# Kernel tuning notes

Measured on AMD Instinct MI355X. Metric: run time of the kernel, lower is better.

## Reference

```python
import jax, jax.numpy as jnp
import numpy as np

B, M, D, H, F, N = 8, 1024, 1024, 16, 4096, 4
DK = D // H
EPS = 1e-5


def _ln(x, g, b):
    mu = jnp.mean(x, axis=-1, keepdims=True)
    var = jnp.mean(jnp.square(x - mu), axis=-1, keepdims=True)
    return (x - mu) * jax.lax.rsqrt(var + EPS) * g + b


def setup_inputs() -> dict:
    key = jax.random.key(0)
    ks = jax.random.split(key, 12)
    s = 0.02
    return {
        "embeds": jax.random.normal(ks[0], (B, M, D), dtype=jnp.float32),
        "weights": jax.random.normal(ks[1], (B, M), dtype=jnp.float32) * 0.1,
        "Wq": jax.random.normal(ks[2], (N, D, D), dtype=jnp.float32) * s,
        "bq": jnp.zeros((N, D), dtype=jnp.float32),
        "Wk": jax.random.normal(ks[3], (N, D, D), dtype=jnp.float32) * s,
        "bk": jnp.zeros((N, D), dtype=jnp.float32),
        "Wv": jax.random.normal(ks[4], (N, D, D), dtype=jnp.float32) * s,
        "bv": jnp.zeros((N, D), dtype=jnp.float32),
        "Wo": jax.random.normal(ks[5], (N, D, D), dtype=jnp.float32) * s,
        "bo": jnp.zeros((N, D), dtype=jnp.float32),
        "W1": jax.random.normal(ks[6], (N, D, F), dtype=jnp.float32) * s,
        "b1": jnp.zeros((N, F), dtype=jnp.float32),
        "W2": jax.random.normal(ks[7], (N, F, D), dtype=jnp.float32) * s,
        "b2": jnp.zeros((N, D), dtype=jnp.float32),
        "g1": jnp.ones((N, D), dtype=jnp.float32),
        "be1": jnp.zeros((N, D), dtype=jnp.float32),
        "g2": jnp.ones((N, D), dtype=jnp.float32),
        "be2": jnp.zeros((N, D), dtype=jnp.float32),
    }


def reference(embeds, weights, Wq, bq, Wk, bk, Wv, bv, Wo, bo,
              W1, b1, W2, b2, g1, be1, g2, be2):
    scale = 1.0 / np.sqrt(DK).astype(np.float32)
    bias = weights[:, None, None, :]  # b,1,1,m additive bias over keys

    def layer(x, p):
        wq, bq_, wk, bk_, wv, bv_, wo, bo_, w1, b1_, w2, b2_, g1_, be1_, g2_, be2_ = p
        q = (x @ wq + bq_).reshape(B, M, H, DK)
        k = (x @ wk + bk_).reshape(B, M, H, DK)
        v = (x @ wv + bv_).reshape(B, M, H, DK)
        scores = jnp.einsum("bqhd,bkhd->bhqk", q, k) * scale + bias
        attn = jax.nn.softmax(scores, axis=-1)
        o = jnp.einsum("bhqk,bkhd->bqhd", attn, v).reshape(B, M, D)
        o = o @ wo + bo_
        x = _ln(x + o, g1_, be1_)
        y = jax.nn.gelu(x @ w1 + b1_, approximate=False) @ w2 + b2_
        x = _ln(x + y, g2_, be2_)
        return x, None

    params = (Wq, bq, Wk, bk, Wv, bv, Wo, bo, W1, b1, W2, b2, g1, be1, g2, be2)
    out, _ = jax.lax.scan(layer, embeds, params)
    return out
```

## Files before the change

kernel.cpp:

```cpp
#include <hip/hip_runtime.h>
#include <hip/hip_bf16.h>

#define BB  8
#define MM  1024
#define DD  1024
#define HH  16
#define FF  4096
#define NL  4
#define DKK 64

typedef __bf16 bf16_t;
typedef __bf16 bf16x8 __attribute__((ext_vector_type(8)));
typedef __bf16 bf16x4 __attribute__((ext_vector_type(4)));
typedef float  f32x4  __attribute__((ext_vector_type(4)));

__device__ __forceinline__ void gld16(const bf16_t* g, bf16_t* l) {
    __builtin_amdgcn_global_load_lds((const __attribute__((address_space(1))) void*)g,
                                     (__attribute__((address_space(3))) void*)l,
                                     16, 0, 0);
}

__global__ __launch_bounds__(256) void cvt_x(const float* __restrict__ e,
                                             float* __restrict__ x,
                                             bf16_t* __restrict__ xb) {
    size_t i = ((size_t)blockIdx.x * 256 + threadIdx.x) * 4;
    float4 v = *(const float4*)(e + i);
    *(float4*)(x + i) = v;
    bf16x4 o;
    o[0] = (bf16_t)v.x; o[1] = (bf16_t)v.y; o[2] = (bf16_t)v.z; o[3] = (bf16_t)v.w;
    *(bf16x4*)(xb + i) = o;
}

__global__ __launch_bounds__(256) void transpose_all(const float* __restrict__ Wq,
                                                     const float* __restrict__ Wk,
                                                     const float* __restrict__ Wv,
                                                     const float* __restrict__ Wo,
                                                     const float* __restrict__ W1,
                                                     const float* __restrict__ W2,
                                                     bf16_t* __restrict__ qkvT,
                                                     bf16_t* __restrict__ WoT,
                                                     bf16_t* __restrict__ W1T,
                                                     bf16_t* __restrict__ W2T) {
    __shared__ float tile[32][33];
    const int bx = blockIdx.x;
    const float* in;
    bf16_t* out;
    int C, t;
    if (bx < 4096) {
        const int mat = bx >> 10;
        t = bx & 1023;
        C = 1024;
        in  = mat == 0 ? Wq : mat == 1 ? Wk : mat == 2 ? Wv : Wo;
        out = mat < 3 ? qkvT + (size_t)mat * DD * DD : WoT;
    } else if (bx < 8192) {
        t = bx - 4096; C = 4096; in = W1; out = W1T;
    } else {
        t = bx - 8192; C = 1024; in = W2; out = W2T;
    }
    const int cb = C >> 5;
    const int c0 = (t % cb) * 32, r0 = (t / cb) * 32;
    const int R = (C == 1024) ? ((bx < 8192) ? 1024 : 4096) : 1024;
    const int tx = threadIdx.x & 31, ty = threadIdx.x >> 5;
    for (int i = 0; i < 4; i++)
        tile[ty + i * 8][tx] = in[(size_t)(r0 + ty + i * 8) * C + c0 + tx];
    __syncthreads();
    for (int i = 0; i < 4; i++)
        out[(size_t)(c0 + ty + i * 8) * R + r0 + tx] = (bf16_t)tile[tx][ty + i * 8];
}

__global__ __launch_bounds__(256) void concat_bias(const float* __restrict__ bq,
                                                   const float* __restrict__ bk,
                                                   const float* __restrict__ bv,
                                                   float* __restrict__ out) {
    const int seg = blockIdx.x, l = blockIdx.y, t = threadIdx.x;
    const float* src = seg == 0 ? bq : seg == 1 ? bk : bv;
    float4 v = *(const float4*)(src + (size_t)l * 1024 + t * 4);
    *(float4*)(out + (size_t)l * 3072 + seg * 1024 + t * 4) = v;
}

__global__ __launch_bounds__(256) void transpose_v_k(const bf16_t* __restrict__ v,
                                                     bf16_t* __restrict__ vT, int ld) {
    __shared__ bf16_t t[64][65];
    int bh = blockIdx.y, b = bh >> 4, h = bh & 15;
    int m0 = blockIdx.x * 64;
    int tx = threadIdx.x & 63, ty = threadIdx.x >> 6;
    for (int i = 0; i < 16; i++) {
        int mr = ty * 16 + i;
        t[mr][tx] = v[(size_t)(b * MM + m0 + mr) * ld + h * DKK + tx];
    }
    __syncthreads();
    for (int i = 0; i < 16; i++) {
        int dk = ty * 16 + i;
        vT[((size_t)(bh * DKK + dk)) * MM + m0 + tx] = t[tx][dk];
    }
}

__device__ __forceinline__ void stage_plane(const bf16_t* __restrict__ G, int K,
                                            size_t rbase, size_t kcol0,
                                            bf16_t* lds, int w, int srow, int scol) {
#pragma unroll
    for (int j = 0; j < 2; j++)
        gld16(G + (rbase + (size_t)(j * 128 + w * 16 + srow)) * (size_t)K + kcol0 + scol,
              lds + j * 4096 + w * 512);
}

template <int EPI>
__global__ __launch_bounds__(512, 2) void gemm256(const bf16_t* __restrict__ A,
                                                  const bf16_t* __restrict__ Bt,
                                                  const float* __restrict__ bias,
                                                  const float* __restrict__ res,
                                                  bf16_t* __restrict__ outb,
                                                  float* __restrict__ outf,
                                                  int K, int Ntot) {
    __shared__ __align__(16) bf16_t As[2 * 2 * 256 * 32];
    __shared__ __align__(16) bf16_t Bs[2 * 2 * 256 * 32];
    const int tid = threadIdx.x, w = tid >> 6, lane = tid & 63;
    const int fr = lane & 15, quad = lane >> 4;
    const int wm = w >> 2, wn = w & 3;
    const int srow = lane >> 2;
    const int scol = ((lane & 3) ^ ((lane >> 3) & 3)) << 3;
    const int swz  = (quad ^ ((fr >> 1) & 3)) << 3;

    const int gx = gridDim.x;
    int lid = blockIdx.y * gx + blockIdx.x;
    {
        const int nwg = gx * gridDim.y;
        const int qq = nwg >> 3, rr = nwg & 7, xc = lid & 7, lq = lid >> 3;
        lid = (xc < rr ? xc * (qq + 1) : rr * (qq + 1) + (xc - rr) * qq) + lq;
    }
    const size_t bm = (size_t)(lid / gx) * 256;
    const size_t bn = (size_t)(lid % gx) * 256;

    const int NT = K >> 6;
    f32x4 acc[8][4] = {};

    stage_plane(A,  K, bm, 0,  As,         w, srow, scol);
    stage_plane(Bt, K, bn, 0,  Bs,         w, srow, scol);
    stage_plane(A,  K, bm, 32, As + 8192,  w, srow, scol);
    stage_plane(Bt, K, bn, 32, Bs + 8192,  w, srow, scol);
    stage_plane(A,  K, bm, 64, As + 16384, w, srow, scol);
    stage_plane(Bt, K, bn, 64, Bs + 16384, w, srow, scol);
    asm volatile("s_waitcnt vmcnt(8)\n\ts_barrier" ::: "memory");

    auto phase = [&](int rdbase, int stbase, size_t stk) {
        bf16x8 af[8], bfv[4];
        const bf16_t* Ap = As + rdbase;
        const bf16_t* Bp = Bs + rdbase;
#pragma unroll
        for (int i = 0; i < 8; i++)
            af[i] = *(const bf16x8*)&Ap[(wm * 128 + i * 16 + fr) * 32 + swz];
#pragma unroll
        for (int j = 0; j < 4; j++)
            bfv[j] = *(const bf16x8*)&Bp[(wn * 64 + j * 16 + fr) * 32 + swz];
        stage_plane(A,  K, bm, stk, As + stbase, w, srow, scol);
        stage_plane(Bt, K, bn, stk, Bs + stbase, w, srow, scol);
        asm volatile("s_barrier" ::: "memory");
        __builtin_amdgcn_s_setprio(1);
#pragma unroll
        for (int i = 0; i < 8; i++)
#pragma unroll
            for (int j = 0; j < 4; j++)
                acc[i][j] = __builtin_amdgcn_mfma_f32_16x16x32_bf16(af[i], bfv[j],
                                                                    acc[i][j], 0, 0, 0);
        __builtin_amdgcn_s_setprio(0);
        asm volatile("s_waitcnt vmcnt(8)\n\ts_barrier" ::: "memory");
    };

    for (int t = 0; t < NT; t += 2) {
        const size_t t1 = (t + 1 < NT) ? t + 1 : NT - 1;
        const size_t t2 = (t + 2 < NT) ? t + 2 : NT - 1;
        const size_t t3 = (t + 3 < NT) ? t + 3 : NT - 1;
        phase(0,     24576, t1 * 64 + 32);
        phase(8192,  0,     t2 * 64);
        phase(16384, 8192,  t2 * 64 + 32);
        phase(24576, 16384, t3 * 64);
    }

#pragma unroll
    for (int j = 0; j < 4; j++) {
        const size_t c = bn + wn * 64 + j * 16 + fr;
        const float bv = bias[c];
#pragma unroll
        for (int i = 0; i < 8; i++) {
            const size_t rbase = bm + wm * 128 + i * 16 + quad * 4;
#pragma unroll
            for (int r = 0; r < 4; r++) {
                const size_t idx = (rbase + r) * (size_t)Ntot + c;
                float v = acc[i][j][r] + bv;
                if constexpr (EPI == 0) {
                    outb[idx] = (bf16_t)v;
                } else if constexpr (EPI == 1) {
                    outf[idx] = v + res[idx];
                } else {
                    float g = 0.5f * v * (1.0f + erff(v * 0.70710678118654752f));
                    outb[idx] = (bf16_t)g;
                }
            }
        }
    }
}

__global__ __launch_bounds__(256) void flash_attn(const bf16_t* __restrict__ q,
                                                  const bf16_t* __restrict__ kmat,
                                                  const bf16_t* __restrict__ vT,
                                                  const float* __restrict__ wts,
                                                  bf16_t* __restrict__ ao, int ldq) {
    __shared__ bf16_t Ks[128 * 72];
    __shared__ bf16_t Vs[64 * 136];
    bf16_t* Ps = Ks;

    const int tid = threadIdx.x;
    const int wave = tid >> 6, lane = tid & 63;
    const int fr = lane & 15, quad = lane >> 4;
    const int fk = quad * 8;
    const int bh = blockIdx.y, b = bh >> 4, h = bh & 15;
    const int q0 = blockIdx.x * 64;

    const size_t qrow = (size_t)(b * MM + q0 + wave * 16 + fr) * ldq + h * DKK;
    const bf16x8 aq0 = *(const bf16x8*)(q + qrow + fk);
    const bf16x8 aq1 = *(const bf16x8*)(q + qrow + 32 + fk);

    f32x4 oacc[4] = {};
    float lrow[4] = {0.f, 0.f, 0.f, 0.f};

    for (int kt = 0; kt < MM; kt += 128) {
        __syncthreads();
#pragma unroll
        for (int rr = 0; rr < 4; rr++) {
            const int key = rr * 32 + (tid >> 3);
            const int dkc = (tid & 7) * 8;
            *(bf16x8*)(&Ks[key * 72 + dkc]) =
                *(const bf16x8*)(kmat + (size_t)(b * MM + kt + key) * ldq + h * DKK + dkc);
            const int dkr = rr * 16 + (tid >> 4);
            const int kc = (tid & 15) * 8;
            *(bf16x8*)(&Vs[dkr * 136 + kc]) =
                *(const bf16x8*)(vT + (size_t)(bh * DKK + dkr) * MM + kt + kc);
        }
        __syncthreads();

        f32x4 s[8];
#pragma unroll
        for (int ni = 0; ni < 8; ni++) {
            const bf16_t* kp = &Ks[(ni * 16 + fr) * 72];
            f32x4 z = {0.f, 0.f, 0.f, 0.f};
            z = __builtin_amdgcn_mfma_f32_16x16x32_bf16(aq0, *(const bf16x8*)(kp + fk), z, 0, 0, 0);
            z = __builtin_amdgcn_mfma_f32_16x16x32_bf16(aq1, *(const bf16x8*)(kp + 32 + fk), z, 0, 0, 0);
            const float wv = wts[b * MM + kt + ni * 16 + fr];
#pragma unroll
            for (int r = 0; r < 4; r++) s[ni][r] = __expf(z[r] * 0.125f + wv);
        }

        float rs[4] = {0.f, 0.f, 0.f, 0.f};
#pragma unroll
        for (int ni = 0; ni < 8; ni++)
#pragma unroll
            for (int r = 0; r < 4; r++) rs[r] += s[ni][r];
#pragma unroll
        for (int off = 1; off < 16; off <<= 1)
#pragma unroll
            for (int r = 0; r < 4; r++) rs[r] += __shfl_xor(rs[r], off, 16);
#pragma unroll
        for (int r = 0; r < 4; r++) lrow[r] += rs[r];

        __syncthreads();

#pragma unroll
        for (int ni = 0; ni < 8; ni++)
#pragma unroll
            for (int r = 0; r < 4; r++)
                Ps[(wave * 16 + quad * 4 + r) * 136 + ni * 16 + fr] = (bf16_t)s[ni][r];

#pragma unroll
        for (int c2 = 0; c2 < 4; c2++) {
            const bf16x8 ap = *(const bf16x8*)(&Ps[(wave * 16 + fr) * 136 + c2 * 32 + fk]);
#pragma unroll
            for (int ni = 0; ni < 4; ni++) {
                const bf16x8 bv = *(const bf16x8*)(&Vs[(ni * 16 + fr) * 136 + c2 * 32 + fk]);
                oacc[ni] = __builtin_amdgcn_mfma_f32_16x16x32_bf16(ap, bv, oacc[ni], 0, 0, 0);
            }
        }
    }

    const size_t orow = (size_t)(b * MM + q0 + wave * 16 + quad * 4);
#pragma unroll
    for (int ni = 0; ni < 4; ni++)
#pragma unroll
        for (int r = 0; r < 4; r++) {
            const float ov = oacc[ni][r] / lrow[r];
            ao[(orow + r) * DD + h * DKK + ni * 16 + fr] = (bf16_t)ov;
        }
}

__global__ __launch_bounds__(256) void ln_k(const float* __restrict__ in,
                                            const float* __restrict__ g,
                                            const float* __restrict__ be,
                                            float* __restrict__ xout,
                                            bf16_t* __restrict__ xb) {
    const int row = blockIdx.x, t = threadIdx.x;
    const float* rp = in + (size_t)row * DD;
    float4 v = *(const float4*)(rp + t * 4);
    float s = v.x + v.y + v.z + v.w;
    float ss = v.x * v.x + v.y * v.y + v.z * v.z + v.w * v.w;
    for (int off = 1; off < 64; off <<= 1) {
        s += __shfl_xor(s, off);
        ss += __shfl_xor(ss, off);
    }
    __shared__ float sb[4], ssb[4];
    if ((t & 63) == 0) { sb[t >> 6] = s; ssb[t >> 6] = ss; }
    __syncthreads();
    s = sb[0] + sb[1] + sb[2] + sb[3];
    ss = ssb[0] + ssb[1] + ssb[2] + ssb[3];
    const float mu = s * (1.0f / DD);
    const float var = ss * (1.0f / DD) - mu * mu;
    const float rstd = rsqrtf(var + 1e-5f);
    float4 gg = *(const float4*)(g + t * 4);
    float4 bb = *(const float4*)(be + t * 4);
    float o0 = (v.x - mu) * rstd * gg.x + bb.x;
    float o1 = (v.y - mu) * rstd * gg.y + bb.y;
    float o2 = (v.z - mu) * rstd * gg.z + bb.z;
    float o3 = (v.w - mu) * rstd * gg.w + bb.w;
    *(float4*)(xout + (size_t)row * DD + t * 4) = make_float4(o0, o1, o2, o3);
    bf16x4 ob;
    ob[0] = (bf16_t)o0; ob[1] = (bf16_t)o1; ob[2] = (bf16_t)o2; ob[3] = (bf16_t)o3;
    *(bf16x4*)(xb + (size_t)row * DD + t * 4) = ob;
}

extern "C" void kernel_launch(void* const* d_in, const int* in_sizes, int n_in,
                              void* d_out, int out_size, void* d_ws, size_t ws_size,
                              hipStream_t stream) {
    const float* embeds = (const float*)d_in[0];
    const float* wts    = (const float*)d_in[1];
    const float* Wq = (const float*)d_in[2];
    const float* bq = (const float*)d_in[3];
    const float* Wk = (const float*)d_in[4];
    const float* bk = (const float*)d_in[5];
    const float* Wv = (const float*)d_in[6];
    const float* bv = (const float*)d_in[7];
    const float* Wo = (const float*)d_in[8];
    const float* bo = (const float*)d_in[9];
    const float* W1 = (const float*)d_in[10];
    const float* b1 = (const float*)d_in[11];
    const float* W2 = (const float*)d_in[12];
    const float* b2 = (const float*)d_in[13];
    const float* g1 = (const float*)d_in[14];
    const float* be1 = (const float*)d_in[15];
    const float* g2 = (const float*)d_in[16];
    const float* be2 = (const float*)d_in[17];
    float* x = (float*)d_out;

    char* p = (char*)d_ws;
    auto take = [&](size_t n) { char* r = p; p += (n + 255) & ~(size_t)255; return r; };
    const size_t nBMD = (size_t)BB * MM * DD;
    bf16_t* xb   = (bf16_t*)take(nBMD * 2);
    bf16_t* qkvb = (bf16_t*)take(nBMD * 3 * 2);
    bf16_t* vTb  = (bf16_t*)take(nBMD * 2);
    float*  r1   = (float*)take(nBMD * 4);
    float*  x1   = (float*)take(nBMD * 4);
    bf16_t* hb   = (bf16_t*)take((size_t)BB * MM * FF * 2);
    bf16_t* qkvT = (bf16_t*)take((size_t)3 * DD * DD * 2);
    bf16_t* WoT  = (bf16_t*)take((size_t)DD * DD * 2);
    bf16_t* W1T  = (bf16_t*)take((size_t)DD * FF * 2);
    bf16_t* W2T  = (bf16_t*)take((size_t)DD * FF * 2);
    float*  qkvB = (float*)take((size_t)NL * 3072 * 4);
    bf16_t* aob  = hb;
    bf16_t* x1b  = xb;

    cvt_x<<<8192, 256, 0, stream>>>(embeds, x, xb);
    concat_bias<<<dim3(3, NL), 256, 0, stream>>>(bq, bk, bv, qkvB);

    const dim3 gQKV(3072 / 256, (BB * MM) / 256);
    const dim3 gDD(DD / 256, (BB * MM) / 256);
    const dim3 gF1(FF / 256, (BB * MM) / 256);

    for (int l = 0; l < NL; l++) {
        transpose_all<<<12288, 256, 0, stream>>>(
            Wq + (size_t)l * DD * DD, Wk + (size_t)l * DD * DD,
            Wv + (size_t)l * DD * DD, Wo + (size_t)l * DD * DD,
            W1 + (size_t)l * DD * FF, W2 + (size_t)l * FF * DD,
            qkvT, WoT, W1T, W2T);

        gemm256<0><<<gQKV, 512, 0, stream>>>(xb, qkvT, qkvB + (size_t)l * 3072,
                                             nullptr, qkvb, nullptr, DD, 3072);

        transpose_v_k<<<dim3(16, 128), 256, 0, stream>>>(qkvb + 2048, vTb, 3072);
        flash_attn<<<dim3(16, 128), 256, 0, stream>>>(qkvb, qkvb + 1024, vTb, wts, aob, 3072);

        gemm256<1><<<gDD, 512, 0, stream>>>(aob, WoT, bo + (size_t)l * DD, x, nullptr, r1, DD, DD);
        ln_k<<<BB * MM, 256, 0, stream>>>(r1, g1 + (size_t)l * DD, be1 + (size_t)l * DD, x1, x1b);

        gemm256<2><<<gF1, 512, 0, stream>>>(x1b, W1T, b1 + (size_t)l * FF, nullptr, hb, nullptr, DD, FF);
        gemm256<1><<<gDD, 512, 0, stream>>>(hb, W2T, b2 + (size_t)l * DD, x1, nullptr, r1, FF, DD);
        ln_k<<<BB * MM, 256, 0, stream>>>(r1, g2 + (size_t)l * DD, be2 + (size_t)l * DD, x, xb);
    }
}
```

Baseline: 2.319 ms.

## Restructure GEMM into 8-phase K=64 pipeline and split-K the D-output GEMMs

The 256x256 GEMM now stages whole 64-wide K tiles into two LDS slots with an XOR swizzle. Each tile is computed in four quadrant phases that interleave LDS fragment reads, the next tile's global-to-LDS loads and MFMA bursts, separated by barriers. The Wo and W2 GEMMs, which have only 128 output tiles, are launched with split-K=2 along grid z. The second half writes raw partials to a scratch buffer, and the layernorm kernel sums both halves before normalizing. This is meant to fill more CUs on the narrow GEMMs and overlap memory with compute better, at the cost of extra partial-sum traffic and more barriers.

```diff
diff --git a/kernel.cpp b/kernel.cpp
--- a/kernel.cpp
+++ b/kernel.cpp
@@ -95,31 +95,22 @@
     }
 }
 
-__device__ __forceinline__ void stage_plane(const bf16_t* __restrict__ G, int K,
-                                            size_t rbase, size_t kcol0,
-                                            bf16_t* lds, int w, int srow, int scol) {
-#pragma unroll
-    for (int j = 0; j < 2; j++)
-        gld16(G + (rbase + (size_t)(j * 128 + w * 16 + srow)) * (size_t)K + kcol0 + scol,
-              lds + j * 4096 + w * 512);
-}
-
 template <int EPI>
-__global__ __launch_bounds__(512, 2) void gemm256(const bf16_t* __restrict__ A,
-                                                  const bf16_t* __restrict__ Bt,
-                                                  const float* __restrict__ bias,
-                                                  const float* __restrict__ res,
-                                                  bf16_t* __restrict__ outb,
-                                                  float* __restrict__ outf,
-                                                  int K, int Ntot) {
-    __shared__ __align__(16) bf16_t As[2 * 2 * 256 * 32];
-    __shared__ __align__(16) bf16_t Bs[2 * 2 * 256 * 32];
+__global__ __launch_bounds__(512, 2) void gemm8p(const bf16_t* __restrict__ A,
+                                                 const bf16_t* __restrict__ Bt,
+                                                 const float* __restrict__ bias,
+                                                 const float* __restrict__ res,
+                                                 bf16_t* __restrict__ outb,
+                                                 float* __restrict__ outf,
+                                                 float* __restrict__ outf2,
+                                                 int K, int Ntot, int Keff) {
+    __shared__ __align__(16) bf16_t As[2 * 2 * 128 * 64];
+    __shared__ __align__(16) bf16_t Bs[2 * 2 * 128 * 64];
     const int tid = threadIdx.x, w = tid >> 6, lane = tid & 63;
-    const int fr = lane & 15, quad = lane >> 4;
+    const int fr = lane & 15, quad = lane >> 4, e7 = fr & 7;
     const int wm = w >> 2, wn = w & 3;
-    const int srow = lane >> 2;
-    const int scol = ((lane & 3) ^ ((lane >> 3) & 3)) << 3;
-    const int swz  = (quad ^ ((fr >> 1) & 3)) << 3;
+    const int grow = lane >> 3;
+    const int gcol = ((lane & 7) ^ (lane >> 3)) << 3;
 
     const int gx = gridDim.x;
     int lid = blockIdx.y * gx + blockIdx.x;
@@ -130,52 +121,112 @@
     }
     const size_t bm = (size_t)(lid / gx) * 256;
     const size_t bn = (size_t)(lid % gx) * 256;
-
-    const int NT = K >> 6;
+    const size_t kbase = (size_t)blockIdx.z * (size_t)Keff;
+    const int NT = Keff >> 6;
+
     f32x4 acc[8][4] = {};
 
-    stage_plane(A,  K, bm, 0,  As,         w, srow, scol);
-    stage_plane(Bt, K, bn, 0,  Bs,         w, srow, scol);
-    stage_plane(A,  K, bm, 32, As + 8192,  w, srow, scol);
-    stage_plane(Bt, K, bn, 32, Bs + 8192,  w, srow, scol);
-    stage_plane(A,  K, bm, 64, As + 16384, w, srow, scol);
-    stage_plane(Bt, K, bn, 64, Bs + 16384, w, srow, scol);
-    asm volatile("s_waitcnt vmcnt(8)\n\ts_barrier" ::: "memory");
-
-    auto phase = [&](int rdbase, int stbase, size_t stk) {
-        bf16x8 af[8], bfv[4];
-        const bf16_t* Ap = As + rdbase;
-        const bf16_t* Bp = Bs + rdbase;
-#pragma unroll
-        for (int i = 0; i < 8; i++)
-            af[i] = *(const bf16x8*)&Ap[(wm * 128 + i * 16 + fr) * 32 + swz];
-#pragma unroll
-        for (int j = 0; j < 4; j++)
-            bfv[j] = *(const bf16x8*)&Bp[(wn * 64 + j * 16 + fr) * 32 + swz];
-        stage_plane(A,  K, bm, stk, As + stbase, w, srow, scol);
-        stage_plane(Bt, K, bn, stk, Bs + stbase, w, srow, scol);
-        asm volatile("s_barrier" ::: "memory");
+    auto stage_half = [&](const bf16_t* __restrict__ G, size_t rowbase, size_t kcol,
+                          bf16_t* dst) {
+#pragma unroll
+        for (int g = 0; g < 2; g++)
+            gld16(G + (rowbase + (size_t)(w * 16 + g * 8 + grow)) * (size_t)K + kcol + gcol,
+                  dst + (w * 16 + g * 8) * 64);
+    };
+    auto stageA = [&](int slot, int tile) {
+        const size_t kc = kbase + (size_t)tile * 64;
+        stage_half(A, bm,       kc, As + slot * 16384);
+        stage_half(A, bm + 128, kc, As + slot * 16384 + 8192);
+    };
+    auto stageB = [&](int slot, int tile) {
+        const size_t kc = kbase + (size_t)tile * 64;
+        stage_half(Bt, bn,       kc, Bs + slot * 16384);
+        stage_half(Bt, bn + 128, kc, Bs + slot * 16384 + 8192);
+    };
+
+    auto aread = [&](int slot, int i, int s) {
+        return *(const bf16x8*)&As[slot * 16384 + wm * 8192 + (i * 16 + fr) * 64 +
+                                   ((((s << 2) | quad) ^ e7) << 3)];
+    };
+    auto bread = [&](int slot, int j, int s) {
+        return *(const bf16x8*)&Bs[slot * 16384 + (wn >> 1) * 8192 +
+                                   ((wn & 1) * 64 + j * 16 + fr) * 64 +
+                                   ((((s << 2) | quad) ^ e7) << 3)];
+    };
+
+    stageA(0, 0); stageB(0, 0);
+    stageA(1, 1); stageB(1, 1);
+    asm volatile("s_waitcnt vmcnt(8)" ::: "memory");
+    __builtin_amdgcn_s_barrier();
+
+    bf16x8 af[4][2], bl[2][2], bh[2][2];
+    for (int T = 0; T < NT; T++) {
+        const int slot = T & 1;
+        const bool st = (T + 2) < NT;
+#pragma unroll
+        for (int i = 0; i < 4; i++) { af[i][0] = aread(slot, i, 0); af[i][1] = aread(slot, i, 1); }
+#pragma unroll
+        for (int j = 0; j < 2; j++) { bl[j][0] = bread(slot, j, 0); bl[j][1] = bread(slot, j, 1); }
+        __builtin_amdgcn_s_barrier();
         __builtin_amdgcn_s_setprio(1);
 #pragma unroll
-        for (int i = 0; i < 8; i++)
-#pragma unroll
-            for (int j = 0; j < 4; j++)
-                acc[i][j] = __builtin_amdgcn_mfma_f32_16x16x32_bf16(af[i], bfv[j],
-                                                                    acc[i][j], 0, 0, 0);
+        for (int i = 0; i < 4; i++)
+#pragma unroll
+            for (int j = 0; j < 2; j++)
+#pragma unroll
+                for (int s = 0; s < 2; s++)
+                    acc[i][j] = __builtin_amdgcn_mfma_f32_16x16x32_bf16(af[i][s], bl[j][s],
+                                                                        acc[i][j], 0, 0, 0);
         __builtin_amdgcn_s_setprio(0);
-        asm volatile("s_waitcnt vmcnt(8)\n\ts_barrier" ::: "memory");
-    };
-
-    for (int t = 0; t < NT; t += 2) {
-        const size_t t1 = (t + 1 < NT) ? t + 1 : NT - 1;
-        const size_t t2 = (t + 2 < NT) ? t + 2 : NT - 1;
-        const size_t t3 = (t + 3 < NT) ? t + 3 : NT - 1;
-        phase(0,     24576, t1 * 64 + 32);
-        phase(8192,  0,     t2 * 64);
-        phase(16384, 8192,  t2 * 64 + 32);
-        phase(24576, 16384, t3 * 64);
-    }
-
+        __builtin_amdgcn_s_barrier();
+#pragma unroll
+        for (int j = 0; j < 2; j++) { bh[j][0] = bread(slot, 2 + j, 0); bh[j][1] = bread(slot, 2 + j, 1); }
+        __builtin_amdgcn_s_barrier();
+        __builtin_amdgcn_s_setprio(1);
+#pragma unroll
+        for (int i = 0; i < 4; i++)
+#pragma unroll
+            for (int j = 0; j < 2; j++)
+#pragma unroll
+                for (int s = 0; s < 2; s++)
+                    acc[i][2 + j] = __builtin_amdgcn_mfma_f32_16x16x32_bf16(af[i][s], bh[j][s],
+                                                                            acc[i][2 + j], 0, 0, 0);
+        __builtin_amdgcn_s_setprio(0);
+        __builtin_amdgcn_s_barrier();
+#pragma unroll
+        for (int i = 0; i < 4; i++) { af[i][0] = aread(slot, 4 + i, 0); af[i][1] = aread(slot, 4 + i, 1); }
+        if (st) stageB(slot, T + 2);
+        __builtin_amdgcn_s_barrier();
+        __builtin_amdgcn_s_setprio(1);
+#pragma unroll
+        for (int i = 0; i < 4; i++)
+#pragma unroll
+            for (int j = 0; j < 2; j++)
+#pragma unroll
+                for (int s = 0; s < 2; s++)
+                    acc[4 + i][2 + j] = __builtin_amdgcn_mfma_f32_16x16x32_bf16(af[i][s], bh[j][s],
+                                                                                acc[4 + i][2 + j], 0, 0, 0);
+        __builtin_amdgcn_s_setprio(0);
+        __builtin_amdgcn_s_barrier();
+        if (st) stageA(slot, T + 2);
+        __builtin_amdgcn_s_barrier();
+        __builtin_amdgcn_s_setprio(1);
+#pragma unroll
+        for (int i = 0; i < 4; i++)
+#pragma unroll
+            for (int j = 0; j < 2; j++)
+#pragma unroll
+                for (int s = 0; s < 2; s++)
+                    acc[4 + i][j] = __builtin_amdgcn_mfma_f32_16x16x32_bf16(af[i][s], bl[j][s],
+                                                                            acc[4 + i][j], 0, 0, 0);
+        __builtin_amdgcn_s_setprio(0);
+        if (st) asm volatile("s_waitcnt vmcnt(8)" ::: "memory");
+        else    asm volatile("s_waitcnt vmcnt(0)" ::: "memory");
+        __builtin_amdgcn_s_barrier();
+    }
+    asm volatile("s_waitcnt vmcnt(0)" ::: "memory");
+
+    const bool raw = (EPI == 1) && (blockIdx.z != 0);
 #pragma unroll
     for (int j = 0; j < 4; j++) {
         const size_t c = bn + wn * 64 + j * 16 + fr;
@@ -186,14 +237,15 @@
 #pragma unroll
             for (int r = 0; r < 4; r++) {
                 const size_t idx = (rbase + r) * (size_t)Ntot + c;
-                float v = acc[i][j][r] + bv;
+                const float a = acc[i][j][r];
                 if constexpr (EPI == 0) {
-                    outb[idx] = (bf16_t)v;
+                    outb[idx] = (bf16_t)(a + bv);
                 } else if constexpr (EPI == 1) {
-                    outf[idx] = v + res[idx];
+                    if (raw) outf2[idx] = a;
+                    else     outf[idx] = a + bv + res[idx];
                 } else {
-                    float g = 0.5f * v * (1.0f + erff(v * 0.70710678118654752f));
-                    outb[idx] = (bf16_t)g;
+                    const float v = a + bv;
+                    outb[idx] = (bf16_t)(0.5f * v * (1.0f + erff(v * 0.70710678118654752f)));
                 }
             }
         }
@@ -291,14 +343,19 @@
         }
 }
 
-__global__ __launch_bounds__(256) void ln_k(const float* __restrict__ in,
+template <bool TWO>
+__global__ __launch_bounds__(256) void ln_t(const float* __restrict__ in,
+                                            const float* __restrict__ in2,
                                             const float* __restrict__ g,
                                             const float* __restrict__ be,
                                             float* __restrict__ xout,
                                             bf16_t* __restrict__ xb) {
     const int row = blockIdx.x, t = threadIdx.x;
-    const float* rp = in + (size_t)row * DD;
-    float4 v = *(const float4*)(rp + t * 4);
+    float4 v = *(const float4*)(in + (size_t)row * DD + t * 4);
+    if constexpr (TWO) {
+        float4 v2 = *(const float4*)(in2 + (size_t)row * DD + t * 4);
+        v.x += v2.x; v.y += v2.y; v.z += v2.z; v.w += v2.w;
+    }
     float s = v.x + v.y + v.z + v.w;
     float ss = v.x * v.x + v.y * v.y + v.z * v.z + v.w * v.w;
     for (int off = 1; off < 64; off <<= 1) {
@@ -364,13 +421,15 @@
     float*  qkvB = (float*)take((size_t)NL * 3072 * 4);
     bf16_t* aob  = hb;
     bf16_t* x1b  = xb;
+    float*  r1b  = (float*)qkvb;
 
     cvt_x<<<8192, 256, 0, stream>>>(embeds, x, xb);
     concat_bias<<<dim3(3, NL), 256, 0, stream>>>(bq, bk, bv, qkvB);
 
     const dim3 gQKV(3072 / 256, (BB * MM) / 256);
-    const dim3 gDD(DD / 256, (BB * MM) / 256);
+    const dim3 gWo(DD / 256, (BB * MM) / 256, 2);
     const dim3 gF1(FF / 256, (BB * MM) / 256);
+    const dim3 gF2(DD / 256, (BB * MM) / 256, 2);
 
     for (int l = 0; l < NL; l++) {
         transpose_all<<<12288, 256, 0, stream>>>(
@@ -379,17 +438,22 @@
             W1 + (size_t)l * DD * FF, W2 + (size_t)l * FF * DD,
             qkvT, WoT, W1T, W2T);
 
-        gemm256<0><<<gQKV, 512, 0, stream>>>(xb, qkvT, qkvB + (size_t)l * 3072,
-                                             nullptr, qkvb, nullptr, DD, 3072);
+        gemm8p<0><<<gQKV, 512, 0, stream>>>(xb, qkvT, qkvB + (size_t)l * 3072,
+                                            nullptr, qkvb, nullptr, nullptr, DD, 3072, DD);
 
         transpose_v_k<<<dim3(16, 128), 256, 0, stream>>>(qkvb + 2048, vTb, 3072);
         flash_attn<<<dim3(16, 128), 256, 0, stream>>>(qkvb, qkvb + 1024, vTb, wts, aob, 3072);
 
-        gemm256<1><<<gDD, 512, 0, stream>>>(aob, WoT, bo + (size_t)l * DD, x, nullptr, r1, DD, DD);
-        ln_k<<<BB * MM, 256, 0, stream>>>(r1, g1 + (size_t)l * DD, be1 + (size_t)l * DD, x1, x1b);
-
-        gemm256<2><<<gF1, 512, 0, stream>>>(x1b, W1T, b1 + (size_t)l * FF, nullptr, hb, nullptr, DD, FF);
-        gemm256<1><<<gDD, 512, 0, stream>>>(hb, W2T, b2 + (size_t)l * DD, x1, nullptr, r1, FF, DD);
-        ln_k<<<BB * MM, 256, 0, stream>>>(r1, g2 + (size_t)l * DD, be2 + (size_t)l * DD, x, xb);
-    }
-}
+        gemm8p<1><<<gWo, 512, 0, stream>>>(aob, WoT, bo + (size_t)l * DD, x,
+                                           nullptr, r1, r1b, DD, DD, DD / 2);
+        ln_t<true><<<BB * MM, 256, 0, stream>>>(r1, r1b, g1 + (size_t)l * DD,
+                                                be1 + (size_t)l * DD, x1, x1b);
+
+        gemm8p<2><<<gF1, 512, 0, stream>>>(x1b, W1T, b1 + (size_t)l * FF,
+                                           nullptr, hb, nullptr, nullptr, DD, FF, DD);
+        gemm8p<1><<<gF2, 512, 0, stream>>>(hb, W2T, b2 + (size_t)l * DD, x1,
+                                           nullptr, r1, r1b, FF, DD, FF / 2);
+        ln_t<true><<<BB * MM, 256, 0, stream>>>(r1, r1b, g2 + (size_t)l * DD,
+                                                be2 + (size_t)l * DD, x, xb);
+    }
+}
```

Measured after the change: 2.393 ms. +3.2%, slower.
